# Performance work log

Hardware: AMD Instinct MI355X
Metric: run time of the kernel (lower is better)

Reference implementation:

```python
import jax, jax.numpy as jnp
import numpy as np


def setup_inputs() -> dict:
    key = jax.random.key(0)
    k1, k2, k3, k4, k5, k6 = jax.random.split(key, 6)
    Bsz, Cin, Cout, H, W = 8, 64, 64, 64, 64
    low_level_feat = jax.random.normal(k1, (Bsz, Cin, H, W), dtype=jnp.float32)
    high_level_feat = jax.random.normal(k2, (Bsz, Cin, H, W), dtype=jnp.float32)
    # 1x1 conv weights == per-pixel channel matmul
    W_low = jax.random.normal(k3, (Cout, Cin), dtype=jnp.float32) * (1.0 / np.sqrt(Cin))
    b_low = jax.random.normal(k4, (Cout,), dtype=jnp.float32) * 0.01
    W_high = jax.random.normal(k5, (Cout, Cin), dtype=jnp.float32) * (1.0 / np.sqrt(Cin))
    b_high = jax.random.normal(k6, (Cout,), dtype=jnp.float32) * 0.01
    return {
        "low_level_feat": low_level_feat,
        "high_level_feat": high_level_feat,
        "W_low": W_low,
        "b_low": b_low,
        "W_high": W_high,
        "b_high": b_high,
    }


def _conv1x1(x, W, b):
    # x: [B, Cin, H, W]; W: [Cout, Cin]; b: [Cout]
    return jnp.einsum('oi,bihw->bohw', W, x) + b[None, :, None, None]


def reference(low_level_feat, high_level_feat, W_low, b_low, W_high, b_high):
    A = _conv1x1(low_level_feat, W_low, b_low)          # [B, C, H, W]
    Bf = _conv1x1(high_level_feat, W_high, b_high)      # [B, C, H, W]
    Bsz, C, H, W = A.shape
    N = H * W
    P = A.reshape(Bsz, C, N)        # [B, C, N]
    Qf = Bf.reshape(Bsz, C, N)      # [B, C, N] (Q in torch is its transpose)
    # S[b,i,j] = sum_c Bf[b,c,i] * A[b,c,j]
    S = jnp.einsum('bci,bcj->bij', Qf, P)               # [B, N, N]
    S = jax.nn.softmax(S, axis=-1)
    # L[b,c,i] = sum_j Bf[b,c,j] * S[b,i,j]
    L = jnp.einsum('bcj,bij->bci', Qf, S)               # [B, C, N]
    O = Bf + L.reshape(Bsz, C, H, W)
    return O
```

## Files before the change

### kernel.cpp

```cpp
#include <hip/hip_runtime.h>
#include <hip/hip_bf16.h>
#include <stdint.h>

#define BATCH 8
#define NPOS 4096
#define LOG2E 1.4426950408889634f

typedef __attribute__((ext_vector_type(4)))  float f32x4;
typedef __attribute__((ext_vector_type(16))) float f32x16;
typedef __attribute__((ext_vector_type(8)))  short bf16x8;

#if __has_builtin(__builtin_amdgcn_exp2f)
#define EXP2(x) __builtin_amdgcn_exp2f(x)
#else
#define EXP2(x) exp2f(x)
#endif

#define SOFTMAX_FENCE() __builtin_amdgcn_sched_barrier(0x3F8)

__device__ __forceinline__ unsigned short bf_rne(float f) {
    unsigned u = __float_as_uint(f);
    u += 0x7fffu + ((u >> 16) & 1u);
    return (unsigned short)(u >> 16);
}
__device__ __forceinline__ unsigned cvt_pk_bf16(float lo, float hi) {
    unsigned r;
    asm("v_cvt_pk_bf16_f32 %0, %1, %2" : "=v"(r) : "v"(lo), "v"(hi));
    return r;
}
__device__ __forceinline__ void permswap32(unsigned &a, unsigned &b) {
    asm volatile("v_permlane32_swap_b32 %0, %1" : "+v"(a), "+v"(b));
}

__global__ __launch_bounds__(64)
void conv_prep(const float* __restrict__ xlow, const float* __restrict__ xhigh,
               const float* __restrict__ Wl, const float* __restrict__ bl,
               const float* __restrict__ Wh, const float* __restrict__ bh,
               unsigned short* __restrict__ KThi, unsigned short* __restrict__ QThi,
               unsigned short* __restrict__ Vc, float* __restrict__ R32)
{
    const int id   = blockIdx.x;
    const int b    = id & 7;
    const int rest = id >> 3;
    const int nb   = rest & 63;
    const int pass = (rest >> 6) & 1;
    const int oq   = rest >> 7;
    const int t    = threadIdx.x;
    const int n    = nb * 64 + t;
    const int o0   = oq * 16;

    const float* __restrict__ x    = pass ? xhigh : xlow;
    const float* __restrict__ W    = pass ? Wh : Wl;
    const float* __restrict__ bias = pass ? bh : bl;

    float xr[64];
#pragma unroll
    for (int i = 0; i < 64; ++i)
        xr[i] = x[((size_t)(b * 64 + i)) * NPOS + n];

    unsigned hpack[8];
#pragma unroll
    for (int oo = 0; oo < 16; ++oo) {
        const int o = o0 + oo;
        float acc = bias[o];
#pragma unroll
        for (int i = 0; i < 64; ++i)
            acc = fmaf(W[o * 64 + i], xr[i], acc);

        if (pass) {
            Vc [((size_t)(b * 64 + o)) * NPOS + n] = bf_rne(acc);
            R32[((size_t)(b * 64 + o)) * NPOS + n] = acc;
        }
        unsigned short h = bf_rne(pass ? acc * LOG2E : acc);
        if (oo & 1) hpack[oo >> 1] |= ((unsigned)h) << 16;
        else        hpack[oo >> 1]  = h;
    }

    unsigned short* dh = pass ? QThi : KThi;
    uint4* ph = (uint4*)(dh + ((size_t)(b * NPOS + n)) * 64 + o0);
#pragma unroll
    for (int q = 0; q < 2; ++q) {
        uint4 v; v.x = hpack[4*q]; v.y = hpack[4*q+1]; v.z = hpack[4*q+2]; v.w = hpack[4*q+3];
        ph[q] = v;
    }
}

__device__ __forceinline__ void stage_st(const unsigned short* __restrict__ KThi,
                                         const unsigned short* __restrict__ Vc,
                                         int b, int j0, char* dst, int w, int lane)
{
#pragma unroll
    for (int q = 0; q < 2; ++q) {
        const int S = w * 2 + q;
        const unsigned short* src;
        if (S < 8) {
            const int it  = S >> 2;
            const int E   = ((S & 3) << 6) | lane;
            const int row = E >> 3, c = E & 7;
            src = KThi + ((size_t)b * NPOS + j0 + it * 32 + row) * 64 + ((c ^ (row & 7)) << 3);
        } else {
            const int E   = ((S - 8) << 6) | lane;
            const int row = E >> 3, c = E & 7;
            src = Vc + ((size_t)(b * 64 + row)) * NPOS + j0 + ((c ^ (row & 7)) << 3);
        }
        __builtin_amdgcn_global_load_lds(
            (const __attribute__((address_space(1))) unsigned int*)(const void*)src,
            (__attribute__((address_space(3))) unsigned int*)(void*)(dst + S * 1024),
            16, 0, 0);
    }
}

__global__ __launch_bounds__(512, 4)
void attn_fused(const unsigned short* __restrict__ KThi,
                const unsigned short* __restrict__ QThi,
                const unsigned short* __restrict__ Vc,
                unsigned short* __restrict__ Pacc, float* __restrict__ Lp,
                int nsplit)
{
    const int id   = blockIdx.x;
    const int b    = id & 7;
    const int qb   = (id >> 3) & 15;
    const int s    = id >> 7;
    const int tid  = threadIdx.x;
    const int w    = tid >> 6;
    const int lane = tid & 63;
    const int r31  = lane & 31;
    const int g2   = lane >> 5;

    const int st0 = (64 * s) / nsplit;
    const int nst = (64 * (s + 1)) / nsplit - st0;

    __shared__ __align__(1024) char smem[32768];

    const int qrow = qb * 256 + w * 32 + r31;
    bf16x8 qhi[4];
#pragma unroll
    for (int kk = 0; kk < 4; ++kk)
        qhi[kk] = *(const bf16x8*)(QThi + ((size_t)b * NPOS + qrow) * 64 + kk * 16 + g2 * 8);

    f32x16 accO0, accO1;
#pragma unroll
    for (int r = 0; r < 16; ++r) { accO0[r] = 0.f; accO1[r] = 0.f; }
    float l_run = 0.f;

    stage_st(KThi, Vc, b, st0 * 64, smem, w, lane);
    __syncthreads();

    for (int st = 0; st < nst; ++st) {
        char* buf = smem + (st & 1) * 16384;
        if (st + 1 < nst)
            stage_st(KThi, Vc, b, (st0 + st + 1) * 64, smem + ((st + 1) & 1) * 16384, w, lane);

#pragma unroll
        for (int itx = 0; itx < 2; ++itx) {
            const int it = itx ^ (w & 1);

            f32x16 sA;
#pragma unroll
            for (int r = 0; r < 16; ++r) sA[r] = 0.f;
            const char* Kb = buf + it * 4096;
            __builtin_amdgcn_s_setprio(1);
#pragma unroll
            for (int kk = 0; kk < 4; ++kk) {
                const int cb  = (kk << 1) | g2;
                const int off = r31 * 128 + ((cb ^ (r31 & 7)) << 4);
                bf16x8 kh = *(const bf16x8*)(Kb + off);
                sA = __builtin_amdgcn_mfma_f32_32x32x16_bf16(kh, qhi[kk], sA, 0, 0, 0);
            }
            __builtin_amdgcn_s_setprio(0);

            unsigned wpk[8];
            float lr0 = 0.f, lr1 = 0.f;
#pragma unroll
            for (int h = 0; h < 8; ++h) {
                float pa = EXP2(sA[2 * h]);
                float pb = EXP2(sA[2 * h + 1]);
                wpk[h] = cvt_pk_bf16(pa, pb);
                lr0 += pa;
                lr1 += pb;
                if (h & 1) SOFTMAX_FENCE();
            }
            l_run += lr0 + lr1;

            unsigned a0 = wpk[0], b0 = wpk[2]; permswap32(a0, b0);
            unsigned a1 = wpk[1], b1 = wpk[3]; permswap32(a1, b1);
            unsigned a2 = wpk[4], b2 = wpk[6]; permswap32(a2, b2);
            unsigned a3 = wpk[5], b3 = wpk[7]; permswap32(a3, b3);
            union { unsigned u[4]; bf16x8 v; } fa0, fa1;
            fa0.u[0] = a0; fa0.u[1] = a1; fa0.u[2] = b0; fa0.u[3] = b1;
            fa1.u[0] = a2; fa1.u[1] = a3; fa1.u[2] = b2; fa1.u[3] = b3;

            __builtin_amdgcn_s_setprio(1);
            {
                const int ch = r31;
                const int c0 = (((it * 2 + 0) << 1) | g2) ^ (ch & 7);
                const int c1 = (((it * 2 + 1) << 1) | g2) ^ (ch & 7);
                bf16x8 vf0 = *(const bf16x8*)(buf + 8192 + ch * 128 + (c0 << 4));
                bf16x8 vf1 = *(const bf16x8*)(buf + 8192 + ch * 128 + (c1 << 4));
                accO0 = __builtin_amdgcn_mfma_f32_32x32x16_bf16(vf0, fa0.v, accO0, 0, 0, 0);
                accO0 = __builtin_amdgcn_mfma_f32_32x32x16_bf16(vf1, fa1.v, accO0, 0, 0, 0);
            }
            {
                const int ch = 32 + r31;
                const int c0 = (((it * 2 + 0) << 1) | g2) ^ (ch & 7);
                const int c1 = (((it * 2 + 1) << 1) | g2) ^ (ch & 7);
                bf16x8 vf0 = *(const bf16x8*)(buf + 8192 + ch * 128 + (c0 << 4));
                bf16x8 vf1 = *(const bf16x8*)(buf + 8192 + ch * 128 + (c1 << 4));
                accO1 = __builtin_amdgcn_mfma_f32_32x32x16_bf16(vf0, fa0.v, accO1, 0, 0, 0);
                accO1 = __builtin_amdgcn_mfma_f32_32x32x16_bf16(vf1, fa1.v, accO1, 0, 0, 0);
            }
            __builtin_amdgcn_s_setprio(0);
        }
        __syncthreads();
    }

    const float l_tot = l_run + __shfl_xor(l_run, 32, 64);
#pragma unroll
    for (int r = 0; r < 16; ++r) {
        const int d0 = (r & 3) + 8 * (r >> 2) + 4 * g2;
        Pacc[(size_t)id * 16384 + (size_t)d0 * 256 + w * 32 + r31]        = bf_rne(accO0[r]);
        Pacc[(size_t)id * 16384 + (size_t)(d0 + 32) * 256 + w * 32 + r31] = bf_rne(accO1[r]);
    }
    if (g2 == 0)
        Lp[(size_t)id * 256 + w * 32 + r31] = l_tot;
}

__global__ __launch_bounds__(256)
void attn_combine(const unsigned short* __restrict__ Pacc, const float* __restrict__ Lp,
                  const float* __restrict__ R32, float* __restrict__ out, int nsplit)
{
    const int cid     = blockIdx.x;
    const int quarter = cid & 3;
    const int b       = (cid >> 2) & 7;
    const int qb      = cid >> 5;
    const int t       = threadIdx.x;

    __shared__ float invL[256];

    {
        float L = 0.f;
        for (int s = 0; s < nsplit; ++s)
            L += Lp[(size_t)((s << 7) | (qb << 3) | b) * 256 + t];
        invL[t] = 1.0f / L;
    }
    __syncthreads();

    const int c_loc = t >> 4;
    const int c     = quarter * 16 + c_loc;
    const int q0    = (t & 15) * 16;

    float acc[16];
#pragma unroll
    for (int i = 0; i < 16; ++i) acc[i] = 0.f;

    for (int s = 0; s < nsplit; ++s) {
        const size_t p = (size_t)((s << 7) | (qb << 3) | b);
        const bf16x8* pp = (const bf16x8*)(Pacc + p * 16384 + (size_t)c * 256 + q0);
#pragma unroll
        for (int h = 0; h < 2; ++h) {
            bf16x8 v = pp[h];
#pragma unroll
            for (int e = 0; e < 8; ++e)
                acc[h * 8 + e] += __uint_as_float(((unsigned)(unsigned short)v[e]) << 16);
        }
    }

    const size_t obase = ((size_t)(b * 64 + c)) * NPOS + qb * 256 + q0;
#pragma unroll
    for (int hv = 0; hv < 4; ++hv) {
        f32x4 rv = *(const f32x4*)(R32 + obase + hv * 4);
        f32x4 v;
#pragma unroll
        for (int e = 0; e < 4; ++e)
            v[e] = acc[hv * 4 + e] * invL[q0 + hv * 4 + e] + rv[e];
        *(f32x4*)(out + obase + hv * 4) = v;
    }
}

extern "C" void kernel_launch(void* const* d_in, const int* in_sizes, int n_in,
                              void* d_out, int out_size, void* d_ws, size_t ws_size,
                              hipStream_t stream)
{
    const float* xlow  = (const float*)d_in[0];
    const float* xhigh = (const float*)d_in[1];
    const float* Wl    = (const float*)d_in[2];
    const float* bl    = (const float*)d_in[3];
    const float* Wh    = (const float*)d_in[4];
    const float* bh    = (const float*)d_in[5];

    char* ws = (char*)d_ws;
    unsigned short* KThi = (unsigned short*)(ws);
    unsigned short* QThi = (unsigned short*)(ws + ( 4u << 20));
    unsigned short* Vc   = (unsigned short*)(ws + ( 8u << 20));
    float*          R32  = (float*)         (ws + (12u << 20));

    const size_t base = (size_t)21u << 20;
    int nsplit = 8;
    while (nsplit > 1) {
        size_t nblk = (size_t)128 * nsplit;
        size_t need = base + nblk * 16384 * 2 + nblk * 256 * 4;
        if (need <= ws_size) break;
        nsplit >>= 1;
    }
    const size_t nblk = (size_t)128 * nsplit;
    unsigned short* Pacc = (unsigned short*)(ws + base);
    float*          Lp   = (float*)(ws + base + nblk * 16384 * 2);

    conv_prep<<<dim3(4096), dim3(64), 0, stream>>>(
        xlow, xhigh, Wl, bl, Wh, bh, KThi, QThi, Vc, R32);
    attn_fused<<<dim3((unsigned)nblk), dim3(512), 0, stream>>>(
        KThi, QThi, Vc, Pacc, Lp, nsplit);
    attn_combine<<<dim3(512), dim3(256), 0, stream>>>(
        Pacc, Lp, R32, (float*)d_out, nsplit);
}
```

Baseline: 84.48 us.

## Pre-swizzle K and V into MFMA fragment layout; load V directly from global

conv_prep now writes K and V in a layout already arranged as MFMA operand fragments, so each lane reads one contiguous 16-byte chunk per fragment. The attention kernel stages only K through LDS and reads V fragments straight from global/L2 into registers, which halves the shared-memory footprint and removes the XOR-swizzle address math. The risk is that V loads are now exposed global latency inside the inner loop rather than being prefetched by the double-buffered LDS stage. The conv_prep V stores also become scattered 2-byte writes.

Measured after the change: 80.90 us. -4.2%, faster.

```diff
diff --git a/kernel.cpp b/kernel.cpp
--- a/kernel.cpp
+++ b/kernel.cpp
@@ -32,12 +32,13 @@
     asm volatile("v_permlane32_swap_b32 %0, %1" : "+v"(a), "+v"(b));
 }
 
+
 __global__ __launch_bounds__(64)
 void conv_prep(const float* __restrict__ xlow, const float* __restrict__ xhigh,
                const float* __restrict__ Wl, const float* __restrict__ bl,
                const float* __restrict__ Wh, const float* __restrict__ bh,
-               unsigned short* __restrict__ KThi, unsigned short* __restrict__ QThi,
-               unsigned short* __restrict__ Vc, float* __restrict__ R32)
+               unsigned short* __restrict__ KF, unsigned short* __restrict__ QThi,
+               unsigned short* __restrict__ VF, float* __restrict__ R32)
 {
     const int id   = blockIdx.x;
     const int b    = id & 7;
@@ -58,6 +59,10 @@
     for (int i = 0; i < 64; ++i)
         xr[i] = x[((size_t)(b * 64 + i)) * NPOS + n];
 
+    char* vbase = (char*)VF + ((size_t)b << 19) + nb * 8192 + ((t >> 5) & 1) * 4096
+                + (oq >> 1) * 2048 + ((t >> 4) & 1) * 1024 + ((t >> 3) & 1) * 512
+                + (oq & 1) * 256 + (t & 7) * 2;
+
     unsigned hpack[8];
 #pragma unroll
     for (int oo = 0; oo < 16; ++oo) {
@@ -68,7 +73,7 @@
             acc = fmaf(W[o * 64 + i], xr[i], acc);
 
         if (pass) {
-            Vc [((size_t)(b * 64 + o)) * NPOS + n] = bf_rne(acc);
+            *(unsigned short*)(vbase + oo * 16) = bf_rne(acc);
             R32[((size_t)(b * 64 + o)) * NPOS + n] = acc;
         }
         unsigned short h = bf_rne(pass ? acc * LOG2E : acc);
@@ -76,44 +81,36 @@
         else        hpack[oo >> 1]  = h;
     }
 
-    unsigned short* dh = pass ? QThi : KThi;
-    uint4* ph = (uint4*)(dh + ((size_t)(b * NPOS + n)) * 64 + o0);
-#pragma unroll
-    for (int q = 0; q < 2; ++q) {
-        uint4 v; v.x = hpack[4*q]; v.y = hpack[4*q+1]; v.z = hpack[4*q+2]; v.w = hpack[4*q+3];
-        ph[q] = v;
-    }
-}
-
-__device__ __forceinline__ void stage_st(const unsigned short* __restrict__ KThi,
-                                         const unsigned short* __restrict__ Vc,
-                                         int b, int j0, char* dst, int w, int lane)
-{
-#pragma unroll
-    for (int q = 0; q < 2; ++q) {
-        const int S = w * 2 + q;
-        const unsigned short* src;
-        if (S < 8) {
-            const int it  = S >> 2;
-            const int E   = ((S & 3) << 6) | lane;
-            const int row = E >> 3, c = E & 7;
-            src = KThi + ((size_t)b * NPOS + j0 + it * 32 + row) * 64 + ((c ^ (row & 7)) << 3);
-        } else {
-            const int E   = ((S - 8) << 6) | lane;
-            const int row = E >> 3, c = E & 7;
-            src = Vc + ((size_t)(b * 64 + row)) * NPOS + j0 + ((c ^ (row & 7)) << 3);
-        }
-        __builtin_amdgcn_global_load_lds(
-            (const __attribute__((address_space(1))) unsigned int*)(const void*)src,
-            (__attribute__((address_space(3))) unsigned int*)(void*)(dst + S * 1024),
-            16, 0, 0);
-    }
+    if (pass) {
+        uint4* ph = (uint4*)(QThi + ((size_t)(b * NPOS + n)) * 64 + o0);
+        uint4 v0; v0.x = hpack[0]; v0.y = hpack[1]; v0.z = hpack[2]; v0.w = hpack[3];
+        uint4 v1; v1.x = hpack[4]; v1.y = hpack[5]; v1.z = hpack[6]; v1.w = hpack[7];
+        ph[0] = v0; ph[1] = v1;
+    } else {
+        char* kbase = (char*)KF + ((size_t)b << 19) + nb * 8192 + ((t >> 5) & 1) * 4096
+                    + oq * 1024 + (t & 31) * 16;
+        uint4 v0; v0.x = hpack[0]; v0.y = hpack[1]; v0.z = hpack[2]; v0.w = hpack[3];
+        uint4 v1; v1.x = hpack[4]; v1.y = hpack[5]; v1.z = hpack[6]; v1.w = hpack[7];
+        *(uint4*)kbase         = v0;
+        *(uint4*)(kbase + 512) = v1;
+    }
+}
+
+__device__ __forceinline__ void stage_k(const unsigned short* __restrict__ KF,
+                                        int b, int st, char* dst, int w, int lane)
+{
+    const char* src = (const char*)KF + ((size_t)b << 19) + (size_t)st * 8192
+                    + w * 1024 + lane * 16;
+    __builtin_amdgcn_global_load_lds(
+        (const __attribute__((address_space(1))) unsigned int*)(const void*)src,
+        (__attribute__((address_space(3))) unsigned int*)(void*)(dst + w * 1024),
+        16, 0, 0);
 }
 
 __global__ __launch_bounds__(512, 4)
-void attn_fused(const unsigned short* __restrict__ KThi,
+void attn_fused(const unsigned short* __restrict__ KF,
                 const unsigned short* __restrict__ QThi,
-                const unsigned short* __restrict__ Vc,
+                const unsigned short* __restrict__ VF,
                 unsigned short* __restrict__ Pacc, float* __restrict__ Lp,
                 int nsplit)
 {
@@ -130,7 +127,7 @@
     const int st0 = (64 * s) / nsplit;
     const int nst = (64 * (s + 1)) / nsplit - st0;
 
-    __shared__ __align__(1024) char smem[32768];
+    __shared__ __align__(1024) char smem[16384];
 
     const int qrow = qb * 256 + w * 32 + r31;
     bf16x8 qhi[4];
@@ -143,13 +140,13 @@
     for (int r = 0; r < 16; ++r) { accO0[r] = 0.f; accO1[r] = 0.f; }
     float l_run = 0.f;
 
-    stage_st(KThi, Vc, b, st0 * 64, smem, w, lane);
+    stage_k(KF, b, st0, smem, w, lane);
     __syncthreads();
 
     for (int st = 0; st < nst; ++st) {
-        char* buf = smem + (st & 1) * 16384;
+        char* buf = smem + (st & 1) * 8192;
         if (st + 1 < nst)
-            stage_st(KThi, Vc, b, (st0 + st + 1) * 64, smem + ((st + 1) & 1) * 16384, w, lane);
+            stage_k(KF, b, st0 + st + 1, smem + ((st + 1) & 1) * 8192, w, lane);
 
 #pragma unroll
         for (int itx = 0; itx < 2; ++itx) {
@@ -162,12 +159,17 @@
             __builtin_amdgcn_s_setprio(1);
 #pragma unroll
             for (int kk = 0; kk < 4; ++kk) {
-                const int cb  = (kk << 1) | g2;
-                const int off = r31 * 128 + ((cb ^ (r31 & 7)) << 4);
-                bf16x8 kh = *(const bf16x8*)(Kb + off);
+                bf16x8 kh = *(const bf16x8*)(Kb + kk * 1024 + lane * 16);
                 sA = __builtin_amdgcn_mfma_f32_32x32x16_bf16(kh, qhi[kk], sA, 0, 0, 0);
             }
             __builtin_amdgcn_s_setprio(0);
+
+            const char* vbase = (const char*)VF + ((size_t)b << 19)
+                              + (size_t)(st0 + st) * 8192 + it * 4096 + lane * 16;
+            bf16x8 vf00 = *(const bf16x8*)(vbase);
+            bf16x8 vf01 = *(const bf16x8*)(vbase + 1024);
+            bf16x8 vf10 = *(const bf16x8*)(vbase + 2048);
+            bf16x8 vf11 = *(const bf16x8*)(vbase + 3072);
 
             unsigned wpk[8];
             float lr0 = 0.f, lr1 = 0.f;
@@ -191,24 +193,10 @@
             fa1.u[0] = a2; fa1.u[1] = a3; fa1.u[2] = b2; fa1.u[3] = b3;
 
             __builtin_amdgcn_s_setprio(1);
-            {
-                const int ch = r31;
-                const int c0 = (((it * 2 + 0) << 1) | g2) ^ (ch & 7);
-                const int c1 = (((it * 2 + 1) << 1) | g2) ^ (ch & 7);
-                bf16x8 vf0 = *(const bf16x8*)(buf + 8192 + ch * 128 + (c0 << 4));
-                bf16x8 vf1 = *(const bf16x8*)(buf + 8192 + ch * 128 + (c1 << 4));
-                accO0 = __builtin_amdgcn_mfma_f32_32x32x16_bf16(vf0, fa0.v, accO0, 0, 0, 0);
-                accO0 = __builtin_amdgcn_mfma_f32_32x32x16_bf16(vf1, fa1.v, accO0, 0, 0, 0);
-            }
-            {
-                const int ch = 32 + r31;
-                const int c0 = (((it * 2 + 0) << 1) | g2) ^ (ch & 7);
-                const int c1 = (((it * 2 + 1) << 1) | g2) ^ (ch & 7);
-                bf16x8 vf0 = *(const bf16x8*)(buf + 8192 + ch * 128 + (c0 << 4));
-                bf16x8 vf1 = *(const bf16x8*)(buf + 8192 + ch * 128 + (c1 << 4));
-                accO1 = __builtin_amdgcn_mfma_f32_32x32x16_bf16(vf0, fa0.v, accO1, 0, 0, 0);
-                accO1 = __builtin_amdgcn_mfma_f32_32x32x16_bf16(vf1, fa1.v, accO1, 0, 0, 0);
-            }
+            accO0 = __builtin_amdgcn_mfma_f32_32x32x16_bf16(vf00, fa0.v, accO0, 0, 0, 0);
+            accO0 = __builtin_amdgcn_mfma_f32_32x32x16_bf16(vf01, fa1.v, accO0, 0, 0, 0);
+            accO1 = __builtin_amdgcn_mfma_f32_32x32x16_bf16(vf10, fa0.v, accO1, 0, 0, 0);
+            accO1 = __builtin_amdgcn_mfma_f32_32x32x16_bf16(vf11, fa1.v, accO1, 0, 0, 0);
             __builtin_amdgcn_s_setprio(0);
         }
         __syncthreads();
@@ -289,12 +277,12 @@
     const float* bh    = (const float*)d_in[5];
 
     char* ws = (char*)d_ws;
-    unsigned short* KThi = (unsigned short*)(ws);
+    unsigned short* KF   = (unsigned short*)(ws);
     unsigned short* QThi = (unsigned short*)(ws + ( 4u << 20));
-    unsigned short* Vc   = (unsigned short*)(ws + ( 8u << 20));
+    unsigned short* VF   = (unsigned short*)(ws + ( 8u << 20));
     float*          R32  = (float*)         (ws + (12u << 20));
 
-    const size_t base = (size_t)21u << 20;
+    const size_t base = (size_t)20u << 20;
     int nsplit = 8;
     while (nsplit > 1) {
         size_t nblk = (size_t)128 * nsplit;
@@ -307,9 +295,9 @@
     float*          Lp   = (float*)(ws + base + nblk * 16384 * 2);
 
     conv_prep<<<dim3(4096), dim3(64), 0, stream>>>(
-        xlow, xhigh, Wl, bl, Wh, bh, KThi, QThi, Vc, R32);
+        xlow, xhigh, Wl, bl, Wh, bh, KF, QThi, VF, R32);
     attn_fused<<<dim3((unsigned)nblk), dim3(512), 0, stream>>>(
-        KThi, QThi, Vc, Pacc, Lp, nsplit);
+        KF, QThi, VF, Pacc, Lp, nsplit);
     attn_combine<<<dim3(512), dim3(256), 0, stream>>>(
         Pacc, Lp, R32, (float*)d_out, nsplit);
 }
```
